# Optimization experiments

Measured on AMD Instinct MI355X. Metric: run time of the kernel, lower is better.

The kernel has to match this reference:

```python
import jax, jax.numpy as jnp
import numpy as np

B, T = 64, 1000
RNN_DIM, EMB_DIM, ATT_DIM, LOC_DIM, KSIZE = 1024, 512, 128, 32, 31


def setup_inputs() -> dict:
    key = jax.random.key(0)
    ks = jax.random.split(key, 8)
    s = 0.02  # small init scale for weights
    return {
        "attention_hidden_state": jax.random.normal(ks[0], (B, RNN_DIM), jnp.float32),
        "memory": jax.random.normal(ks[1], (B, T, EMB_DIM), jnp.float32),
        "processed_memory": jax.random.normal(ks[2], (B, T, ATT_DIM), jnp.float32),
        "attention_weights_cat": jax.random.uniform(ks[3], (B, 2, T), jnp.float32),
        "mask": jnp.zeros((B, T), dtype=bool),
        "W_query": jax.random.normal(ks[4], (ATT_DIM, RNN_DIM), jnp.float32) * s,
        "conv_w": jax.random.normal(ks[5], (LOC_DIM, 2, KSIZE), jnp.float32) * s,
        "W_loc": jax.random.normal(ks[6], (ATT_DIM, LOC_DIM), jnp.float32) * s,
        "v": jax.random.normal(ks[7], (1, ATT_DIM), jnp.float32) * s,
    }


def reference(attention_hidden_state, memory, processed_memory,
              attention_weights_cat, mask, W_query, conv_w, W_loc, v):
    # processed_query: (B, 1, ATT_DIM)
    pq = (attention_hidden_state @ W_query.T)[:, None, :]
    # location features: conv1d over (B, 2, T), SAME padding, no bias
    loc = jax.lax.conv_general_dilated(
        attention_weights_cat, conv_w,
        window_strides=(1,), padding="SAME",
        dimension_numbers=("NCH", "OIH", "NCH"))  # (B, LOC_DIM, T)
    loc = jnp.einsum("bct,ac->bta", loc, W_loc)  # (B, T, ATT_DIM)
    # energies: v . tanh(pq + loc + processed_memory) -> (B, T)
    energy = jnp.einsum("bta,oa->bt", jnp.tanh(pq + loc + processed_memory), v)
    energy = jnp.where(mask, -jnp.inf, energy)
    attention_weights = jax.nn.softmax(energy, axis=1)  # (B, T)
    attention_context = jnp.einsum("bt,bte->be", attention_weights, memory)
    return attention_context, attention_weights
```

## Files before the change

kernel.cpp:

```cpp
#include <hip/hip_runtime.h>
#include <hip/hip_bf16.h>
#include <math.h>

#define B 64
#define T 1000
#define RNN_DIM 1024
#define EMB_DIM 512
#define ATT_DIM 128
#define LOC_DIM 32
#define KSIZE 31
#define PAD 15
#define ET 64
#define CHUNK 40

__global__ __launch_bounds__(256) void pq_kernel(
    const float* __restrict__ hidden,
    const float* __restrict__ Wq,
    float* __restrict__ pq)
{
    int gwave = (blockIdx.x * blockDim.x + threadIdx.x) >> 6;
    int lane  = threadIdx.x & 63;
    int b = gwave >> 7;
    int a = gwave & 127;

    const float4* h4 = (const float4*)(hidden + (size_t)b * RNN_DIM);
    const float4* w4 = (const float4*)(Wq + (size_t)a * RNN_DIM);

    float acc = 0.f;
#pragma unroll
    for (int j = 0; j < 4; ++j) {
        float4 h = h4[j * 64 + lane];
        float4 w = w4[j * 64 + lane];
        acc += h.x * w.x + h.y * w.y + h.z * w.z + h.w * w.w;
    }
#pragma unroll
    for (int off = 32; off > 0; off >>= 1)
        acc += __shfl_down(acc, off, 64);
    if (lane == 0) pq[gwave] = acc;
}

__global__ __launch_bounds__(256) void energy_kernel(
    const float* __restrict__ aw,
    const float* __restrict__ cw,
    const float* __restrict__ wl,
    const float* __restrict__ pq,
    const float* __restrict__ pm,
    const float* __restrict__ v,
    float* __restrict__ energy)
{
    __shared__ float aw_lds[2][ET + 2 * PAD];
    __shared__ float cw_lds[LOC_DIM][2][KSIZE];
    __shared__ float wl_lds[ATT_DIM][36];
    __shared__ float pq_lds[ATT_DIM];
    __shared__ float v_lds[ATT_DIM];
    __shared__ float loc_lds[ET][36];
    __shared__ float pm_lds[ET][132];

    const int b   = blockIdx.x;
    const int t0  = blockIdx.y * ET;
    const int tid = threadIdx.x;

    const float4* pm4 = (const float4*)(pm + (size_t)b * T * ATT_DIM);
    for (int i = tid; i < ET * 32; i += 256) {
        int t = i >> 5, c4 = i & 31;
        int tt = t0 + t;
        float4 val = make_float4(0.f, 0.f, 0.f, 0.f);
        if (tt < T) val = pm4[(size_t)tt * 32 + c4];
        *((float4*)&pm_lds[t][c4 * 4]) = val;
    }
    for (int i = tid; i < LOC_DIM * 2 * KSIZE; i += 256)
        ((float*)cw_lds)[i] = cw[i];
    for (int i = tid; i < ATT_DIM * LOC_DIM; i += 256)
        wl_lds[i >> 5][i & 31] = wl[i];
    if (tid < ATT_DIM) {
        pq_lds[tid] = pq[b * ATT_DIM + tid];
        v_lds[tid]  = v[tid];
    }
    for (int i = tid; i < 2 * (ET + 2 * PAD); i += 256) {
        int ch = i / (ET + 2 * PAD);
        int p  = i % (ET + 2 * PAD);
        int t  = t0 + p - PAD;
        aw_lds[ch][p] = (t >= 0 && t < T) ? aw[(size_t)b * 2 * T + ch * T + t] : 0.f;
    }
    __syncthreads();

    {
        const int c  = tid & 31;
        const int tg = tid >> 5;
        float acc[8];
#pragma unroll
        for (int j = 0; j < 8; ++j) acc[j] = 0.f;
#pragma unroll
        for (int ch = 0; ch < 2; ++ch) {
            float awr[KSIZE + 7];
#pragma unroll
            for (int j = 0; j < KSIZE + 7; ++j) awr[j] = aw_lds[ch][tg * 8 + j];
#pragma unroll
            for (int k = 0; k < KSIZE; ++k) {
                float cv = cw_lds[c][ch][k];
#pragma unroll
                for (int j = 0; j < 8; ++j) acc[j] += cv * awr[k + j];
            }
        }
#pragma unroll
        for (int j = 0; j < 8; ++j) loc_lds[tg * 8 + j][c] = acc[j];
    }
    __syncthreads();

    {
        const int tl = tid >> 2;
        const int aq = tid & 3;

        float lr[32];
#pragma unroll
        for (int j = 0; j < 8; ++j)
            *((float4*)&lr[4 * j]) = *((const float4*)&loc_lds[tl][4 * j]);

        float acc = 0.f;
#pragma unroll 4
        for (int aa = 0; aa < 32; ++aa) {
            const int a = aq + 4 * aa;
            float e = pq_lds[a] + pm_lds[tl][a];
#pragma unroll
            for (int j = 0; j < 8; ++j) {
                float4 w4 = *((const float4*)&wl_lds[a][4 * j]);
                e += w4.x * lr[4*j] + w4.y * lr[4*j+1] + w4.z * lr[4*j+2] + w4.w * lr[4*j+3];
            }
            float ex = __expf(2.f * e);
            float th = 1.f - 2.f * __builtin_amdgcn_rcpf(1.f + ex);
            acc += v_lds[a] * th;
        }
        acc += __shfl_xor(acc, 1, 64);
        acc += __shfl_xor(acc, 2, 64);
        if (aq == 0 && (t0 + tl) < T)
            energy[b * T + t0 + tl] = acc;
    }
}

__global__ __launch_bounds__(256) void softmax_kernel(
    const float* __restrict__ energy,
    const unsigned char* __restrict__ mask,
    float* __restrict__ out)
{
    int b   = blockIdx.x;
    int tid = threadIdx.x;

    for (int i = tid; i < EMB_DIM; i += 256) out[b * EMB_DIM + i] = 0.f;

    __shared__ float red[4];
    float e[4];
    float mx = -INFINITY;
#pragma unroll
    for (int j = 0; j < 4; ++j) {
        int t = tid + j * 256;
        if (t < T) {
            float val = energy[b * T + t];
            if (mask[b * T + t]) val = -INFINITY;
            e[j] = val;
            mx = fmaxf(mx, val);
        } else e[j] = -INFINITY;
    }
#pragma unroll
    for (int off = 32; off > 0; off >>= 1)
        mx = fmaxf(mx, __shfl_down(mx, off, 64));
    if ((tid & 63) == 0) red[tid >> 6] = mx;
    __syncthreads();
    mx = fmaxf(fmaxf(red[0], red[1]), fmaxf(red[2], red[3]));
    __syncthreads();

    float sum = 0.f;
    float ex[4];
#pragma unroll
    for (int j = 0; j < 4; ++j) {
        ex[j] = (e[j] == -INFINITY) ? 0.f : expf(e[j] - mx);
        sum += ex[j];
    }
#pragma unroll
    for (int off = 32; off > 0; off >>= 1)
        sum += __shfl_down(sum, off, 64);
    if ((tid & 63) == 0) red[tid >> 6] = sum;
    __syncthreads();
    sum = red[0] + red[1] + red[2] + red[3];
    float inv = 1.f / sum;
#pragma unroll
    for (int j = 0; j < 4; ++j) {
        int t = tid + j * 256;
        if (t < T) out[B * EMB_DIM + b * T + t] = ex[j] * inv;
    }
}

__global__ __launch_bounds__(256) void context_kernel(
    const float* __restrict__ memory,
    const float* __restrict__ w,
    float* __restrict__ ctx)
{
    __shared__ float w_lds[CHUNK];
    __shared__ float red[4][EMB_DIM];

    const int b   = blockIdx.x;
    const int t0  = blockIdx.y * CHUNK;
    const int tid = threadIdx.x;
    const int e8  = tid & 63;
    const int ts  = tid >> 6;

    if (tid < CHUNK) w_lds[tid] = w[b * T + t0 + tid];

    const float4* base = (const float4*)(memory + (size_t)b * T * EMB_DIM)
                         + (size_t)t0 * 128 + e8 * 2;

    float4 m0[10], m1[10];
#pragma unroll
    for (int i = 0; i < 10; ++i) {
        const float4* row = base + (size_t)(ts + 4 * i) * 128;
        m0[i] = row[0];
        m1[i] = row[1];
    }
    __syncthreads();

    float4 acc0 = {0.f, 0.f, 0.f, 0.f};
    float4 acc1 = {0.f, 0.f, 0.f, 0.f};
#pragma unroll
    for (int i = 0; i < 10; ++i) {
        float wt = w_lds[ts + 4 * i];
        acc0.x += wt * m0[i].x; acc0.y += wt * m0[i].y;
        acc0.z += wt * m0[i].z; acc0.w += wt * m0[i].w;
        acc1.x += wt * m1[i].x; acc1.y += wt * m1[i].y;
        acc1.z += wt * m1[i].z; acc1.w += wt * m1[i].w;
    }

    float* r = &red[ts][e8 * 8];
    r[0] = acc0.x; r[1] = acc0.y; r[2] = acc0.z; r[3] = acc0.w;
    r[4] = acc1.x; r[5] = acc1.y; r[6] = acc1.z; r[7] = acc1.w;
    __syncthreads();
    for (int i = tid; i < EMB_DIM; i += 256) {
        float s = red[0][i] + red[1][i] + red[2][i] + red[3][i];
        atomicAdd(ctx + b * EMB_DIM + i, s);
    }
}

extern "C" void kernel_launch(void* const* d_in, const int* in_sizes, int n_in,
                              void* d_out, int out_size, void* d_ws, size_t ws_size,
                              hipStream_t stream) {
    const float* hidden = (const float*)d_in[0];
    const float* memory = (const float*)d_in[1];
    const float* pm     = (const float*)d_in[2];
    const float* aw     = (const float*)d_in[3];
    const unsigned char* mask = (const unsigned char*)d_in[4];
    const float* Wq     = (const float*)d_in[5];
    const float* cw     = (const float*)d_in[6];
    const float* wl     = (const float*)d_in[7];
    const float* v      = (const float*)d_in[8];

    float* out = (float*)d_out;

    float* pq_ws     = (float*)d_ws;
    float* energy_ws = pq_ws + B * ATT_DIM;

    pq_kernel<<<dim3((B * ATT_DIM) / 4), dim3(256), 0, stream>>>(hidden, Wq, pq_ws);

    energy_kernel<<<dim3(B, (T + ET - 1) / ET), dim3(256), 0, stream>>>(
        aw, cw, wl, pq_ws, pm, v, energy_ws);

    softmax_kernel<<<dim3(B), dim3(256), 0, stream>>>(energy_ws, mask, out);

    context_kernel<<<dim3(B, T / CHUNK), dim3(256), 0, stream>>>(
        memory, out + B * EMB_DIM, out);
}
```

Before: 266.8 us.

## Register-block energy kernel and split context reduction by embedding slice

The energy kernel now has each thread compute 4 time steps across 8 attention channels. It keeps processed_memory in registers rather than LDS, so each loaded W_loc row is reused across four time steps, and it requests two blocks per CU via launch bounds. The context kernel is reorganized so each block owns a 32-wide embedding slice and loops over all T. This removes the atomicAdd reduction and the zero-initialization in softmax. The trade-offs are higher register pressure, possible spills in the energy kernel, and longer serial loops per block in the context kernel.

Result: slower. 326.2 us (+22.3%).

```diff
diff --git a/kernel.cpp b/kernel.cpp
--- a/kernel.cpp
+++ b/kernel.cpp
@@ -11,7 +11,7 @@
 #define KSIZE 31
 #define PAD 15
 #define ET 64
-#define CHUNK 40
+#define ESL 32
 
 __global__ __launch_bounds__(256) void pq_kernel(
     const float* __restrict__ hidden,
@@ -39,7 +39,7 @@
     if (lane == 0) pq[gwave] = acc;
 }
 
-__global__ __launch_bounds__(256) void energy_kernel(
+__global__ __launch_bounds__(256, 2) void energy_kernel(
     const float* __restrict__ aw,
     const float* __restrict__ cw,
     const float* __restrict__ wl,
@@ -54,20 +54,26 @@
     __shared__ float pq_lds[ATT_DIM];
     __shared__ float v_lds[ATT_DIM];
     __shared__ float loc_lds[ET][36];
-    __shared__ float pm_lds[ET][132];
 
     const int b   = blockIdx.x;
     const int t0  = blockIdx.y * ET;
     const int tid = threadIdx.x;
 
-    const float4* pm4 = (const float4*)(pm + (size_t)b * T * ATT_DIM);
-    for (int i = tid; i < ET * 32; i += 256) {
-        int t = i >> 5, c4 = i & 31;
-        int tt = t0 + t;
-        float4 val = make_float4(0.f, 0.f, 0.f, 0.f);
-        if (tt < T) val = pm4[(size_t)tt * 32 + c4];
-        *((float4*)&pm_lds[t][c4 * 4]) = val;
-    }
+    const int TL = tid >> 4;
+    const int AL = tid & 15;
+    const int tb = TL * 4;
+
+    float pmr[4][8];
+#pragma unroll
+    for (int jj = 0; jj < 4; ++jj) {
+        const int t = t0 + tb + jj;
+        const bool ok = (t < T);
+        const float* prow = pm + ((size_t)b * T + (ok ? t : T - 1)) * ATT_DIM;
+#pragma unroll
+        for (int aa = 0; aa < 8; ++aa)
+            pmr[jj][aa] = ok ? prow[AL + 16 * aa] : 0.f;
+    }
+
     for (int i = tid; i < LOC_DIM * 2 * KSIZE; i += 256)
         ((float*)cw_lds)[i] = cw[i];
     for (int i = tid; i < ATT_DIM * LOC_DIM; i += 256)
@@ -108,32 +114,48 @@
     __syncthreads();
 
     {
-        const int tl = tid >> 2;
-        const int aq = tid & 3;
-
-        float lr[32];
-#pragma unroll
-        for (int j = 0; j < 8; ++j)
-            *((float4*)&lr[4 * j]) = *((const float4*)&loc_lds[tl][4 * j]);
-
-        float acc = 0.f;
-#pragma unroll 4
-        for (int aa = 0; aa < 32; ++aa) {
-            const int a = aq + 4 * aa;
-            float e = pq_lds[a] + pm_lds[tl][a];
-#pragma unroll
-            for (int j = 0; j < 8; ++j) {
-                float4 w4 = *((const float4*)&wl_lds[a][4 * j]);
-                e += w4.x * lr[4*j] + w4.y * lr[4*j+1] + w4.z * lr[4*j+2] + w4.w * lr[4*j+3];
+        float lr[4][32];
+#pragma unroll
+        for (int jj = 0; jj < 4; ++jj)
+#pragma unroll
+            for (int q = 0; q < 8; ++q)
+                *((float4*)&lr[jj][4 * q]) = *((const float4*)&loc_lds[tb + jj][4 * q]);
+
+        float acc[4] = {0.f, 0.f, 0.f, 0.f};
+#pragma unroll
+        for (int aa = 0; aa < 8; ++aa) {
+            const int a = AL + 16 * aa;
+            const float pqa = pq_lds[a];
+            const float va  = v_lds[a];
+            float4 w[8];
+#pragma unroll
+            for (int q = 0; q < 8; ++q)
+                w[q] = *((const float4*)&wl_lds[a][4 * q]);
+#pragma unroll
+            for (int jj = 0; jj < 4; ++jj) {
+                float e = pqa + pmr[jj][aa];
+#pragma unroll
+                for (int q = 0; q < 8; ++q) {
+                    e += w[q].x * lr[jj][4*q]   + w[q].y * lr[jj][4*q+1]
+                       + w[q].z * lr[jj][4*q+2] + w[q].w * lr[jj][4*q+3];
+                }
+                float ex = __expf(2.f * e);
+                float th = 1.f - 2.f * __builtin_amdgcn_rcpf(1.f + ex);
+                acc[jj] += va * th;
             }
-            float ex = __expf(2.f * e);
-            float th = 1.f - 2.f * __builtin_amdgcn_rcpf(1.f + ex);
-            acc += v_lds[a] * th;
-        }
-        acc += __shfl_xor(acc, 1, 64);
-        acc += __shfl_xor(acc, 2, 64);
-        if (aq == 0 && (t0 + tl) < T)
-            energy[b * T + t0 + tl] = acc;
+        }
+#pragma unroll
+        for (int jj = 0; jj < 4; ++jj) {
+            float s = acc[jj];
+            s += __shfl_xor(s, 1, 64);
+            s += __shfl_xor(s, 2, 64);
+            s += __shfl_xor(s, 4, 64);
+            s += __shfl_xor(s, 8, 64);
+            if (AL == 0) {
+                int t = t0 + tb + jj;
+                if (t < T) energy[b * T + t] = s;
+            }
+        }
     }
 }
 
@@ -144,8 +166,6 @@
 {
     int b   = blockIdx.x;
     int tid = threadIdx.x;
-
-    for (int i = tid; i < EMB_DIM; i += 256) out[b * EMB_DIM + i] = 0.f;
 
     __shared__ float red[4];
     float e[4];
@@ -194,47 +214,51 @@
     const float* __restrict__ w,
     float* __restrict__ ctx)
 {
-    __shared__ float w_lds[CHUNK];
-    __shared__ float red[4][EMB_DIM];
+    __shared__ float w_lds[1024];
+    __shared__ float red[4][ESL];
 
     const int b   = blockIdx.x;
-    const int t0  = blockIdx.y * CHUNK;
+    const int e0  = blockIdx.y * ESL;
     const int tid = threadIdx.x;
-    const int e8  = tid & 63;
-    const int ts  = tid >> 6;
-
-    if (tid < CHUNK) w_lds[tid] = w[b * T + t0 + tid];
-
-    const float4* base = (const float4*)(memory + (size_t)b * T * EMB_DIM)
-                         + (size_t)t0 * 128 + e8 * 2;
-
-    float4 m0[10], m1[10];
-#pragma unroll
-    for (int i = 0; i < 10; ++i) {
-        const float4* row = base + (size_t)(ts + 4 * i) * 128;
-        m0[i] = row[0];
-        m1[i] = row[1];
-    }
-    __syncthreads();
-
-    float4 acc0 = {0.f, 0.f, 0.f, 0.f};
-    float4 acc1 = {0.f, 0.f, 0.f, 0.f};
-#pragma unroll
-    for (int i = 0; i < 10; ++i) {
-        float wt = w_lds[ts + 4 * i];
-        acc0.x += wt * m0[i].x; acc0.y += wt * m0[i].y;
-        acc0.z += wt * m0[i].z; acc0.w += wt * m0[i].w;
-        acc1.x += wt * m1[i].x; acc1.y += wt * m1[i].y;
-        acc1.z += wt * m1[i].z; acc1.w += wt * m1[i].w;
-    }
-
-    float* r = &red[ts][e8 * 8];
-    r[0] = acc0.x; r[1] = acc0.y; r[2] = acc0.z; r[3] = acc0.w;
-    r[4] = acc1.x; r[5] = acc1.y; r[6] = acc1.z; r[7] = acc1.w;
-    __syncthreads();
-    for (int i = tid; i < EMB_DIM; i += 256) {
-        float s = red[0][i] + red[1][i] + red[2][i] + red[3][i];
-        atomicAdd(ctx + b * EMB_DIM + i, s);
+    const int col = tid & 7;
+    const int rg  = tid >> 3;
+
+    for (int i = tid; i < 1024; i += 256)
+        w_lds[i] = (i < T) ? w[b * T + i] : 0.f;
+    __syncthreads();
+
+    const float4* mem4 = (const float4*)(memory + (size_t)b * T * EMB_DIM + e0);
+
+    float4 acc = {0.f, 0.f, 0.f, 0.f};
+    float4 mbuf[8];
+#pragma unroll 1
+    for (int blk = 0; blk < 4; ++blk) {
+        const int rbase = blk * 256 + rg;
+#pragma unroll
+        for (int u = 0; u < 8; ++u) {
+            int r  = rbase + 32 * u;
+            int rc = (r < T) ? r : (T - 1);
+            mbuf[u] = mem4[(size_t)rc * 128 + col];
+        }
+#pragma unroll
+        for (int u = 0; u < 8; ++u) {
+            float wt = w_lds[rbase + 32 * u];
+            acc.x += wt * mbuf[u].x; acc.y += wt * mbuf[u].y;
+            acc.z += wt * mbuf[u].z; acc.w += wt * mbuf[u].w;
+        }
+    }
+
+    acc.x += __shfl_xor(acc.x, 8, 64);  acc.x += __shfl_xor(acc.x, 16, 64);  acc.x += __shfl_xor(acc.x, 32, 64);
+    acc.y += __shfl_xor(acc.y, 8, 64);  acc.y += __shfl_xor(acc.y, 16, 64);  acc.y += __shfl_xor(acc.y, 32, 64);
+    acc.z += __shfl_xor(acc.z, 8, 64);  acc.z += __shfl_xor(acc.z, 16, 64);  acc.z += __shfl_xor(acc.z, 32, 64);
+    acc.w += __shfl_xor(acc.w, 8, 64);  acc.w += __shfl_xor(acc.w, 16, 64);  acc.w += __shfl_xor(acc.w, 32, 64);
+
+    if ((tid & 63) < 8)
+        *((float4*)&red[tid >> 6][4 * col]) = acc;
+    __syncthreads();
+    if (tid < ESL) {
+        float s = red[0][tid] + red[1][tid] + red[2][tid] + red[3][tid];
+        ctx[b * EMB_DIM + e0 + tid] = s;
     }
 }
 
@@ -263,6 +287,6 @@
 
     softmax_kernel<<<dim3(B), dim3(256), 0, stream>>>(energy_ws, mask, out);
 
-    context_kernel<<<dim3(B, T / CHUNK), dim3(256), 0, stream>>>(
+    context_kernel<<<dim3(B, EMB_DIM / ESL), dim3(256), 0, stream>>>(
         memory, out + B * EMB_DIM, out);
 }
```
